# Performance work log

Measured on AMD Instinct MI355X. Metric: run time of the kernel, lower is better.

Reference implementation:

```python
import jax, jax.numpy as jnp
import numpy as np
import math

NUM_BANDS = 16
BINS = 1024
CROPSIZE = 1024
BATCH = 4


def setup_inputs() -> dict:
    key = jax.random.key(0)
    ks = jax.random.split(key, 10)
    s = 1.0 / math.sqrt(BINS)
    return {
        "x": jax.random.normal(ks[0], (BATCH, CROPSIZE, BINS), jnp.float32),
        "Wq": jax.random.normal(ks[1], (BINS, BINS), jnp.float32) * s,
        "bq": jax.random.normal(ks[2], (BINS,), jnp.float32) * 0.02,
        "Wk": jax.random.normal(ks[3], (BINS, BINS), jnp.float32) * s,
        "bk": jax.random.normal(ks[4], (BINS,), jnp.float32) * 0.02,
        "Wv": jax.random.normal(ks[5], (BINS, BINS), jnp.float32) * s,
        "bv": jax.random.normal(ks[6], (BINS,), jnp.float32) * 0.02,
        "Wo": jax.random.normal(ks[7], (BINS, BINS), jnp.float32) * s,
        "bo": jax.random.normal(ks[8], (BINS,), jnp.float32) * 0.02,
        "er": jax.random.normal(ks[9], (BINS // NUM_BANDS, CROPSIZE), jnp.float32),
    }


def reference(x, Wq, bq, Wk, bk, Wv, bv, Wo, bo, er):
    b, w, c = x.shape
    h = NUM_BANDS
    d = c // h
    # Linear projections (torch Linear: x @ W.T + b)
    q = (jnp.einsum("bwc,oc->bwo", x, Wq) + bq).reshape(b, w, h, d).transpose(0, 2, 1, 3)  # [b,h,w,d]
    k = (jnp.einsum("bwc,oc->bwo", x, Wk) + bk).reshape(b, w, h, d).transpose(0, 2, 1, 3)  # [b,h,w,d]
    v = (jnp.einsum("bwc,oc->bwo", x, Wv) + bv).reshape(b, w, h, d).transpose(0, 2, 1, 3)  # [b,h,w,d]
    # relative-position bias via skew trick
    qe = jnp.einsum("bhwd,dc->bhwc", q, er)  # [b,h,w,cropsize]
    qe = jnp.pad(qe, ((0, 0), (0, 0), (0, 0), (1, 0)))  # pad last dim on left -> [b,h,w,crop+1]
    p = jnp.swapaxes(qe, 2, 3)[:, :, 1:, :]  # [b,h,crop,w] == [b,h,w,w] since crop==w
    qk = (jnp.einsum("bhwd,bhud->bhwu", q, k) + p) / math.sqrt(c)
    a = jax.nn.softmax(qk, axis=-1)
    av = jnp.einsum("bhwu,bhud->bhwd", a, v).transpose(0, 2, 1, 3).reshape(b, w, c)
    return jnp.einsum("bwc,oc->bwo", av, Wo) + bo
```

## Files before the change

### kernel.cpp

```cpp
#include <hip/hip_runtime.h>
#include <stdint.h>

typedef __attribute__((ext_vector_type(8))) short   short8;
typedef __attribute__((ext_vector_type(8))) __bf16  bf16x8;
typedef __attribute__((ext_vector_type(4))) float   floatx4;

__device__ __forceinline__ float bf2f(uint16_t h) {
    union { uint32_t u; float f; } v; v.u = ((uint32_t)h) << 16; return v.f;
}
__device__ __forceinline__ uint16_t f2bf(float f) {
    union { float f; uint32_t u; } v; v.f = f;
    uint32_t u = v.u;
    u += 0x7FFFu + ((u >> 16) & 1u);
    return (uint16_t)(u >> 16);
}
__device__ __forceinline__ floatx4 mfma16(short8 a, short8 b, floatx4 c) {
    return __builtin_amdgcn_mfma_f32_16x16x32_bf16(
        __builtin_bit_cast(bf16x8, a), __builtin_bit_cast(bf16x8, b), c, 0, 0, 0);
}
__device__ __forceinline__ void gll16(const short* g, short* l) {
    __builtin_amdgcn_global_load_lds(
        (const __attribute__((address_space(1))) uint32_t*)g,
        (__attribute__((address_space(3))) uint32_t*)l, 16, 0, 0);
}

__global__ void conv_all(
    const float* __restrict__ x,
    const float* __restrict__ Wq, const float* __restrict__ Wk,
    const float* __restrict__ Wv, const float* __restrict__ Wo,
    const float* __restrict__ bq, const float* __restrict__ bk,
    const float* __restrict__ bv, const float* __restrict__ bo,
    const float* __restrict__ er,
    short* __restrict__ xb, short* __restrict__ Wb,
    short* __restrict__ ball, short* __restrict__ ErT)
{
    int blk = blockIdx.x, tid = threadIdx.x;
    if (blk < 4096) {
        int i = blk * 256 + tid;
        float4 v = ((const float4*)x)[i];
        ((short4*)xb)[i] = make_short4((short)f2bf(v.x), (short)f2bf(v.y),
                                       (short)f2bf(v.z), (short)f2bf(v.w));
    } else if (blk < 8192) {
        int rel = blk - 4096;
        int wsel = rel >> 10;
        int i = (rel & 1023) * 256 + tid;
        const float* W = (wsel == 0) ? Wq : (wsel == 1) ? Wk : (wsel == 2) ? Wv : Wo;
        float4 v = ((const float4*)W)[i];
        ((short4*)(Wb + ((size_t)wsel << 20)))[i] =
            make_short4((short)f2bf(v.x), (short)f2bf(v.y),
                        (short)f2bf(v.z), (short)f2bf(v.w));
    } else if (blk < 8448) {
        int idx = (blk - 8192) * 256 + tid;
        int w = idx >> 6, d = idx & 63;
        ErT[idx] = (short)f2bf(er[d * 1024 + w]);
    } else {
        int idx = (blk - 8448) * 256 + tid;
        int sel = idx >> 10, j = idx & 1023;
        const float* s = (sel == 0) ? bq : (sel == 1) ? bk : (sel == 2) ? bv : bo;
        ball[idx] = (short)f2bf(s[j]);
    }
}

__device__ __forceinline__ void gemm_body(
    const short* __restrict__ A, const short* __restrict__ Wt,
    const short* __restrict__ bias, short* __restrict__ dst,
    float* __restrict__ dstf, int variant)
{
    __shared__ short As[128 * 64];
    __shared__ short Bs[128 * 64];
    const int tid  = threadIdx.x;
    const int wid  = tid >> 6;
    const int lane = tid & 63;
    const int m0 = blockIdx.x * 128;
    const int n0 = blockIdx.y * 128;
    const int wm = (wid >> 1) * 64;
    const int wn = (wid & 1) * 64;
    const int lrow = lane & 15;
    const int quad = lane >> 4;
    const int srow = lane >> 3;
    const int sscol = (((lane & 7) ^ (srow & 7)) << 3);
    const int rx = lrow & 7;

    floatx4 acc[4][4];
#pragma unroll
    for (int r = 0; r < 4; ++r)
#pragma unroll
        for (int c = 0; c < 4; ++c) acc[r][c] = (floatx4){0.f, 0.f, 0.f, 0.f};

    for (int k0 = 0; k0 < 1024; k0 += 64) {
#pragma unroll
        for (int i = 0; i < 4; ++i) {
            int q = wid * 4 + i;
            gll16(A + (size_t)(m0 + q * 8 + srow) * 1024 + k0 + sscol,
                  &As[q * 512 + lane * 8]);
        }
#pragma unroll
        for (int i = 0; i < 4; ++i) {
            int q = wid * 4 + i;
            gll16(Wt + (size_t)(n0 + q * 8 + srow) * 1024 + k0 + sscol,
                  &Bs[q * 512 + lane * 8]);
        }
        __syncthreads();
#pragma unroll
        for (int ks = 0; ks < 2; ++ks) {
            short8 af[4], bfr[4];
#pragma unroll
            for (int r = 0; r < 4; ++r)
                af[r] = *(const short8*)&As[(wm + r * 16 + lrow) * 64 +
                                            (((ks * 4 + quad) ^ rx) << 3)];
#pragma unroll
            for (int c = 0; c < 4; ++c)
                bfr[c] = *(const short8*)&Bs[(wn + c * 16 + lrow) * 64 +
                                             (((ks * 4 + quad) ^ rx) << 3)];
#pragma unroll
            for (int r = 0; r < 4; ++r)
#pragma unroll
                for (int c = 0; c < 4; ++c)
                    acc[r][c] = mfma16(af[r], bfr[c], acc[r][c]);
        }
        __syncthreads();
    }

#pragma unroll
    for (int c = 0; c < 4; ++c) {
        int col = n0 + wn + c * 16 + lrow;
        float bv = bf2f((uint16_t)bias[col]);
#pragma unroll
        for (int r = 0; r < 4; ++r) {
#pragma unroll
            for (int g = 0; g < 4; ++g) {
                int m = m0 + wm + r * 16 + quad * 4 + g;
                float fv = acc[r][c][g] + bv;
                if (variant == 3) {
                    dstf[(size_t)m * 1024 + col] = fv;
                } else if (variant == 2) {
                    int bh = (m >> 10) * 16 + (col >> 6);
                    dst[(size_t)bh * 65536 + (size_t)(col & 63) * 1024 + (m & 1023)] =
                        (short)f2bf(fv);
                } else {
                    int bh = (m >> 10) * 16 + (col >> 6);
                    dst[(size_t)bh * 65536 + (size_t)(m & 1023) * 64 + (col & 63)] =
                        (short)f2bf(fv);
                }
            }
        }
    }
}

__global__ __launch_bounds__(256) void qkv_gemm(
    const short* __restrict__ x,
    const short* __restrict__ Wb, const short* __restrict__ bqkv,
    short* __restrict__ Qb, short* __restrict__ Kb, short* __restrict__ Vb)
{
    int z = blockIdx.z;
    const short* Wt = Wb + ((size_t)z << 20);
    short* dst      = (z == 0) ? Qb : (z == 1) ? Kb : Vb;
    gemm_body(x, Wt, bqkv + z * 1024, dst, nullptr, z);
}

__global__ __launch_bounds__(256) void out_gemm(
    const short* __restrict__ AV, const short* __restrict__ Wo,
    const short* __restrict__ bo, float* __restrict__ out)
{
    gemm_body(AV, Wo, bo, nullptr, out, 3);
}

#define PSTR 72
__global__ __launch_bounds__(512) void attn_kernel(
    const short* __restrict__ Q, const short* __restrict__ K,
    const short* __restrict__ Vt, const short* __restrict__ ErT,
    short* __restrict__ AV)
{
    __shared__ short Ks [2][64 * 64];
    __shared__ short Qks[2][64 * 64];
    __shared__ short Vs [2][64 * 64];
    __shared__ short Ps [128 * PSTR];
    const int tid  = threadIdx.x;
    const int wid  = tid >> 6;
    const int lane = tid & 63;
    const int lrow = lane & 15;
    const int quad = lane >> 4;
    const int lk   = quad * 8;
    const int srow = lane >> 3;
    const int sscol = (((lane & 7) ^ (srow & 7)) << 3);
    const int rx = lrow & 7;
    const int h = blockIdx.x, b = blockIdx.y;
    const int bh = b * 16 + h;
    const int i0 = blockIdx.z * 128;
    const int wrow = wid * 16;
    const short* Qbh = Q  + (size_t)bh * 65536;
    const short* Kbh = K  + (size_t)bh * 65536;
    const short* Vbh = Vt + (size_t)bh * 65536;

    short8 qa[4];
    {
        int row = i0 + wrow + lrow;
#pragma unroll
        for (int kk = 0; kk < 2; ++kk) {
            qa[kk]     = *(const short8*)&Qbh[(size_t)row * 64 + kk * 32 + lk];
            qa[kk + 2] = *(const short8*)&ErT[(size_t)row * 64 + kk * 32 + lk];
        }
    }

    float lrun[4];
    floatx4 oacc[4];
#pragma unroll
    for (int g = 0; g < 4; ++g) lrun[g] = 0.f;
#pragma unroll
    for (int c = 0; c < 4; ++c) oacc[c] = (floatx4){0.f, 0.f, 0.f, 0.f};

    {
        gll16(Kbh + (size_t)(wid * 8 + srow) * 64 + sscol,    &Ks [0][wid * 512 + lane * 8]);
        gll16(Qbh + (size_t)(wid * 8 + srow) * 64 + sscol,    &Qks[0][wid * 512 + lane * 8]);
        gll16(Vbh + (size_t)(wid * 8 + srow) * 1024 + sscol,  &Vs [0][wid * 512 + lane * 8]);
    }

    const float sc2 = 1.44269504088896f / 32.0f;

    for (int jt = 0; jt < 16; ++jt) {
        const int cur = jt & 1;
        __syncthreads();

        if (jt < 15) {
            int j1 = (jt + 1) * 64;
            gll16(Kbh + (size_t)(j1 + wid * 8 + srow) * 64 + sscol,    &Ks [cur ^ 1][wid * 512 + lane * 8]);
            gll16(Qbh + (size_t)(j1 + wid * 8 + srow) * 64 + sscol,    &Qks[cur ^ 1][wid * 512 + lane * 8]);
            gll16(Vbh + (size_t)(wid * 8 + srow) * 1024 + j1 + sscol,  &Vs [cur ^ 1][wid * 512 + lane * 8]);
        }

        floatx4 s[4];
#pragma unroll
        for (int c = 0; c < 4; ++c) s[c] = (floatx4){0.f, 0.f, 0.f, 0.f};
#pragma unroll
        for (int kk = 0; kk < 4; ++kk) {
            short8 kb[4];
#pragma unroll
            for (int c = 0; c < 4; ++c) {
                int kl = (kk < 2) ? kk : kk - 2;
                const short* src = (kk < 2) ? Ks[cur] : Qks[cur];
                kb[c] = *(const short8*)&src[(c * 16 + lrow) * 64 +
                                             (((kl * 4 + quad) ^ rx) << 3)];
            }
#pragma unroll
            for (int c = 0; c < 4; ++c)
                s[c] = mfma16(qa[kk], kb[c], s[c]);
        }

#pragma unroll
        for (int c = 0; c < 4; ++c)
#pragma unroll
            for (int g = 0; g < 4; ++g)
                s[c][g] = exp2f(s[c][g] * sc2);
#pragma unroll
        for (int g = 0; g < 4; ++g) {
            float rs = (s[0][g] + s[1][g]) + (s[2][g] + s[3][g]);
#pragma unroll
            for (int d = 1; d < 16; d <<= 1) rs += __shfl_xor(rs, d, 64);
            lrun[g] += rs;
        }

#pragma unroll
        for (int c = 0; c < 4; ++c)
#pragma unroll
            for (int g = 0; g < 4; ++g)
                Ps[(wrow + quad * 4 + g) * PSTR + c * 16 + lrow] = (short)f2bf(s[c][g]);
        __asm__ __volatile__("" ::: "memory");

#pragma unroll
        for (int kk = 0; kk < 2; ++kk) {
            short8 pa, vb[4];
            pa = *(const short8*)&Ps[(wrow + lrow) * PSTR + kk * 32 + lk];
#pragma unroll
            for (int c = 0; c < 4; ++c)
                vb[c] = *(const short8*)&Vs[cur][(c * 16 + lrow) * 64 +
                                                 (((kk * 4 + quad) ^ rx) << 3)];
#pragma unroll
            for (int c = 0; c < 4; ++c)
                oacc[c] = mfma16(pa, vb[c], oacc[c]);
        }
    }

#pragma unroll
    for (int c = 0; c < 4; ++c)
#pragma unroll
        for (int g = 0; g < 4; ++g) {
            int row = i0 + wrow + quad * 4 + g;
            int colc = h * 64 + c * 16 + lrow;
            AV[((size_t)b * 1024 + row) * 1024 + colc] = (short)f2bf(oacc[c][g] / lrun[g]);
        }
}

extern "C" void kernel_launch(void* const* d_in, const int* in_sizes, int n_in,
                              void* d_out, int out_size, void* d_ws, size_t ws_size,
                              hipStream_t stream) {
    const float* x  = (const float*)d_in[0];
    const float* Wq = (const float*)d_in[1];
    const float* bq = (const float*)d_in[2];
    const float* Wk = (const float*)d_in[3];
    const float* bk = (const float*)d_in[4];
    const float* Wv = (const float*)d_in[5];
    const float* bv = (const float*)d_in[6];
    const float* Wo = (const float*)d_in[7];
    const float* bo = (const float*)d_in[8];
    const float* er = (const float*)d_in[9];
    float* out = (float*)d_out;

    const size_t M1 = 1u << 20;
    short* ws   = (short*)d_ws;
    short* xb   = (short*)d_out;
    short* Qb   = ws;
    short* Kb   = ws + 4 * M1;
    short* Vb   = ws + 8 * M1;
    short* AVb  = ws + 12 * M1;
    short* Wb   = ws + 16 * M1;
    short* ball = ws + 20 * M1;
    short* ErT  = ws + 20 * M1 + 4096;

    hipLaunchKernelGGL(conv_all, dim3(8464), dim3(256), 0, stream,
                       x, Wq, Wk, Wv, Wo, bq, bk, bv, bo, er, xb, Wb, ball, ErT);
    hipLaunchKernelGGL(qkv_gemm, dim3(32, 8, 3), dim3(256), 0, stream,
                       xb, Wb, ball, Qb, Kb, Vb);
    hipLaunchKernelGGL(attn_kernel, dim3(16, 4, 8), dim3(512), 0, stream,
                       Qb, Kb, Vb, ErT, AVb);
    hipLaunchKernelGGL(out_gemm, dim3(32, 8), dim3(256), 0, stream,
                       AVb, Wb + 3 * M1, ball + 3072, out);
}
```

Measured before the change: 213.9 us.

## Replace QKV GEMM with 256x256-tile 8-wave pipelined kernel

Replaces the QKV projection GEMM with a new kernel that uses 256x256 output tiles, 512 threads, and 128KB dynamic LDS. Global-to-LDS loads are double-buffered and interleaved with MFMA quadrants, with explicit barriers, vmcnt waits, and setprio. The aim is more operand reuse per tile and hidden load latency. The cost is 192 blocks on 256 CUs, which leaves some CUs idle, plus heavy register pressure and many barriers.

```diff
diff --git a/kernel.cpp b/kernel.cpp
--- a/kernel.cpp
+++ b/kernel.cpp
@@ -147,22 +147,160 @@
     }
 }
 
-__global__ __launch_bounds__(256) void qkv_gemm(
-    const short* __restrict__ x,
-    const short* __restrict__ Wb, const short* __restrict__ bqkv,
-    short* __restrict__ Qb, short* __restrict__ Kb, short* __restrict__ Vb)
-{
-    int z = blockIdx.z;
-    const short* Wt = Wb + ((size_t)z << 20);
-    short* dst      = (z == 0) ? Qb : (z == 1) ? Kb : Vb;
-    gemm_body(x, Wt, bqkv + z * 1024, dst, nullptr, z);
-}
-
 __global__ __launch_bounds__(256) void out_gemm(
     const short* __restrict__ AV, const short* __restrict__ Wo,
     const short* __restrict__ bo, float* __restrict__ out)
 {
     gemm_body(AV, Wo, bo, nullptr, out, 3);
+}
+
+#define Q8_BAR   asm volatile("s_barrier" ::: "memory")
+#define Q8_VM4   asm volatile("s_waitcnt vmcnt(4)" ::: "memory")
+#define Q8_VM0   asm volatile("s_waitcnt vmcnt(0)" ::: "memory")
+
+__device__ __forceinline__ void stage_half(const short* src, short* region, int tid)
+{
+    const int lane = tid & 63;
+    const int wid  = tid >> 6;
+    const int srow = lane >> 3;
+    const int scol = (((lane & 7) ^ srow) << 3);
+#pragma unroll
+    for (int round = 0; round < 2; ++round) {
+        int r = round * 64 + wid * 8 + srow;
+        gll16(src + (size_t)r * 1024 + scol,
+              region + round * 4096 + wid * 512 + lane * 8);
+    }
+}
+
+#define SA(buf, h) (As + ((buf) * 2 + (h)) * 8192)
+#define SB(buf, h) (Bs + ((buf) * 2 + (h)) * 8192)
+#define STAGE_A(buf, h, kt) stage_half(Asrc + (size_t)(h) * 131072 + (size_t)(kt) * 64, SA(buf, h), tid)
+#define STAGE_B(buf, h, kt) stage_half(Bsrc + (size_t)(h) * 131072 + (size_t)(kt) * 64, SB(buf, h), tid)
+
+#define READ_A(buf, MQ) do { const short* Rp_ = SA(buf, wm); \
+    _Pragma("unroll") for (int r_ = 0; r_ < 4; ++r_) { \
+        int row_ = (MQ) * 64 + r_ * 16 + lrow; \
+        _Pragma("unroll") for (int ks_ = 0; ks_ < 2; ++ks_) \
+            a[r_][ks_] = *(const short8*)&Rp_[row_ * 64 + (((ks_ * 4 + quad) ^ rx) << 3)]; \
+    } } while (0)
+
+#define READ_B(buf, NQ, BB) do { const short* Rp_ = SB(buf, wn >> 1); \
+    _Pragma("unroll") for (int c_ = 0; c_ < 2; ++c_) { \
+        int row_ = (wn & 1) * 64 + (NQ) * 32 + c_ * 16 + lrow; \
+        _Pragma("unroll") for (int ks_ = 0; ks_ < 2; ++ks_) \
+            BB[c_][ks_] = *(const short8*)&Rp_[row_ * 64 + (((ks_ * 4 + quad) ^ rx) << 3)]; \
+    } } while (0)
+
+#define MFMA_QUAD(MQ, NQ, BB) do { \
+    __builtin_amdgcn_s_setprio(1); \
+    _Pragma("unroll") for (int ks_ = 0; ks_ < 2; ++ks_) \
+        _Pragma("unroll") for (int r_ = 0; r_ < 4; ++r_) \
+            _Pragma("unroll") for (int c_ = 0; c_ < 2; ++c_) \
+                acc[(MQ) * 4 + r_][(NQ) * 2 + c_] = \
+                    mfma16(a[r_][ks_], BB[c_][ks_], acc[(MQ) * 4 + r_][(NQ) * 2 + c_]); \
+    __builtin_amdgcn_s_setprio(0); \
+    } while (0)
+
+__global__ __launch_bounds__(512, 2) void qkv_gemm256(
+    const short* __restrict__ x, const short* __restrict__ Wb,
+    const short* __restrict__ ball,
+    short* __restrict__ Qb, short* __restrict__ Kb, short* __restrict__ Vb)
+{
+    extern __shared__ short lds[];
+    short* As = lds;
+    short* Bs = lds + 32768;
+    const int tid  = threadIdx.x;
+    const int wid  = tid >> 6;
+    const int lane = tid & 63;
+    const int wm   = wid >> 2;
+    const int wn   = wid & 3;
+    const int lrow = lane & 15;
+    const int quad = lane >> 4;
+    const int rx   = lrow & 7;
+    const int m0 = blockIdx.x * 256;
+    const int n0 = blockIdx.y * 256;
+    const short* Asrc = x  + (size_t)m0 * 1024;
+    const short* Bsrc = Wb + (size_t)n0 * 1024;
+
+    floatx4 acc[8][4];
+#pragma unroll
+    for (int r = 0; r < 8; ++r)
+#pragma unroll
+        for (int c = 0; c < 4; ++c) acc[r][c] = (floatx4){0.f, 0.f, 0.f, 0.f};
+
+    short8 a[4][2], b0[2][2], b1[2][2];
+
+    STAGE_A(0, 0, 0); STAGE_A(0, 1, 0); STAGE_B(0, 0, 0); STAGE_B(0, 1, 0);
+    STAGE_B(1, 0, 1); STAGE_B(1, 1, 1);
+    Q8_VM4;
+    Q8_BAR;
+
+#pragma unroll 1
+    for (int i = 0; i < 7; ++i) {
+        const int t1 = 2 * i + 1, s0 = 2 * i + 2, s1 = 2 * i + 3;
+        READ_A(0, 0); READ_B(0, 0, b0);
+        STAGE_A(1, 0, t1);
+        Q8_BAR; MFMA_QUAD(0, 0, b0); Q8_BAR;
+        READ_B(0, 1, b1);
+        STAGE_A(1, 1, t1);
+        Q8_BAR; MFMA_QUAD(0, 1, b1); Q8_BAR;
+        READ_A(0, 1);
+        STAGE_B(0, 0, s0);
+        Q8_BAR; MFMA_QUAD(1, 1, b1); Q8_BAR;
+        STAGE_B(0, 1, s0);
+        Q8_VM4;
+        Q8_BAR; MFMA_QUAD(1, 0, b0); Q8_BAR;
+        READ_A(1, 0); READ_B(1, 0, b0);
+        STAGE_A(0, 0, s0);
+        Q8_BAR; MFMA_QUAD(0, 0, b0); Q8_BAR;
+        READ_B(1, 1, b1);
+        STAGE_A(0, 1, s0);
+        Q8_BAR; MFMA_QUAD(0, 1, b1); Q8_BAR;
+        READ_A(1, 1);
+        STAGE_B(1, 0, s1);
+        Q8_BAR; MFMA_QUAD(1, 1, b1); Q8_BAR;
+        STAGE_B(1, 1, s1);
+        Q8_VM4;
+        Q8_BAR; MFMA_QUAD(1, 0, b0); Q8_BAR;
+    }
+
+    STAGE_A(1, 0, 15); STAGE_A(1, 1, 15);
+    Q8_VM4;
+    Q8_BAR;
+    READ_A(0, 0); READ_B(0, 0, b0); READ_B(0, 1, b1);
+    MFMA_QUAD(0, 0, b0); MFMA_QUAD(0, 1, b1);
+    READ_A(0, 1);
+    MFMA_QUAD(1, 0, b0); MFMA_QUAD(1, 1, b1);
+    Q8_VM0;
+    Q8_BAR;
+    READ_A(1, 0); READ_B(1, 0, b0); READ_B(1, 1, b1);
+    MFMA_QUAD(0, 0, b0); MFMA_QUAD(0, 1, b1);
+    READ_A(1, 1);
+    MFMA_QUAD(1, 0, b0); MFMA_QUAD(1, 1, b1);
+
+    const int z = n0 >> 10;
+    short* dst = (z == 0) ? Qb : (z == 1) ? Kb : Vb;
+#pragma unroll
+    for (int fc = 0; fc < 4; ++fc) {
+        int col = n0 + wn * 64 + fc * 16 + lrow;
+        int c1  = col & 1023;
+        float bv = bf2f((uint16_t)ball[col]);
+#pragma unroll
+        for (int fr = 0; fr < 8; ++fr) {
+#pragma unroll
+            for (int g = 0; g < 4; ++g) {
+                int m = m0 + wm * 128 + fr * 16 + quad * 4 + g;
+                float fv = acc[fr][fc][g] + bv;
+                int bh = (m >> 10) * 16 + (c1 >> 6);
+                if (z == 2)
+                    dst[(size_t)bh * 65536 + (size_t)(c1 & 63) * 1024 + (m & 1023)] =
+                        (short)f2bf(fv);
+                else
+                    dst[(size_t)bh * 65536 + (size_t)(m & 1023) * 64 + (c1 & 63)] =
+                        (short)f2bf(fv);
+            }
+        }
+    }
 }
 
 #define PSTR 72
@@ -316,9 +454,16 @@
     short* ball = ws + 20 * M1;
     short* ErT  = ws + 20 * M1 + 4096;
 
+    static bool attr_done = false;
+    if (!attr_done) {
+        hipFuncSetAttribute((const void*)qkv_gemm256,
+                            hipFuncAttributeMaxDynamicSharedMemorySize, 131072);
+        attr_done = true;
+    }
+
     hipLaunchKernelGGL(conv_all, dim3(8464), dim3(256), 0, stream,
                        x, Wq, Wk, Wv, Wo, bq, bk, bv, bo, er, xb, Wb, ball, ErT);
-    hipLaunchKernelGGL(qkv_gemm, dim3(32, 8, 3), dim3(256), 0, stream,
+    hipLaunchKernelGGL(qkv_gemm256, dim3(16, 12), dim3(512), 131072, stream,
                        xb, Wb, ball, Qb, Kb, Vb);
     hipLaunchKernelGGL(attn_kernel, dim3(16, 4, 8), dim3(512), 0, stream,
                        Qb, Kb, Vb, ErT, AVb);
```

Result: no change. 217.6 us (+1.7%).

## Replace QKV GEMM with 256x192-tile pipelined kernel using direct-to-LDS loads

Applied to the files above, without the earlier changes.

Replaces the per-projection QKV GEMM (grid 32x8x3, 256 threads) with one fused 256x192-tile kernel of 512 threads. It treats the three weight matrices as a single N=3072 problem and launches 256 blocks with a swizzled block order. K-slices are double-buffered in LDS through global_load_lds with XOR swizzling. Manual vmcnt waits and barriers overlap staging of the next slice with MFMA phases, and setprio raises priority during math. The aim is more data reuse per tile, fewer blocks, and better load/compute overlap; the costs are 112KB of dynamic LDS, high register pressure and hand-tuned wait counts.

```diff
diff --git a/kernel.cpp b/kernel.cpp
--- a/kernel.cpp
+++ b/kernel.cpp
@@ -147,22 +147,142 @@
     }
 }
 
-__global__ __launch_bounds__(256) void qkv_gemm(
-    const short* __restrict__ x,
-    const short* __restrict__ Wb, const short* __restrict__ bqkv,
-    short* __restrict__ Qb, short* __restrict__ Kb, short* __restrict__ Vb)
-{
-    int z = blockIdx.z;
-    const short* Wt = Wb + ((size_t)z << 20);
-    short* dst      = (z == 0) ? Qb : (z == 1) ? Kb : Vb;
-    gemm_body(x, Wt, bqkv + z * 1024, dst, nullptr, z);
-}
-
 __global__ __launch_bounds__(256) void out_gemm(
     const short* __restrict__ AV, const short* __restrict__ Wo,
     const short* __restrict__ bo, float* __restrict__ out)
 {
     gemm_body(AV, Wo, bo, nullptr, out, 3);
+}
+
+#define VM7  asm volatile("s_waitcnt vmcnt(7)" ::: "memory")
+#define VM6  asm volatile("s_waitcnt vmcnt(6)" ::: "memory")
+#define VM0  asm volatile("s_waitcnt vmcnt(0)" ::: "memory")
+#define BARR asm volatile("s_barrier" ::: "memory")
+
+__device__ __forceinline__ void stage_unit(const short* src, short* region, int tid)
+{
+    const int row  = tid >> 3;
+    const int scol = (((tid & 7) ^ (row & 7)) << 3);
+    gll16(src + (size_t)row * 1024 + scol, region + tid * 8);
+}
+
+#define SAU(buf, u) (As + (buf) * 16384 + (u) * 4096)
+#define SBU(buf, u) (Bs + (buf) * 12288 + (u) * 4096)
+#define STG_A(buf, u, kt) stage_unit(Asrc + (size_t)(u) * 65536 + (size_t)(kt) * 64, SAU(buf, u), tid)
+#define STG_B(buf, u, kt) stage_unit(Bsrc + (size_t)(u) * 65536 + (size_t)(kt) * 64, SBU(buf, u), tid)
+
+#define RD_A(buf) do { \
+    _Pragma("unroll") for (int fr_ = 0; fr_ < 8; ++fr_) { \
+        const short* p_ = SAU(buf, wm * 2 + (fr_ >> 2)) + ((fr_ & 3) * 16 + lrow) * 64; \
+        _Pragma("unroll") for (int ks_ = 0; ks_ < 2; ++ks_) \
+            a[fr_][ks_] = *(const short8*)&p_[((ks_ * 4 + quad) ^ rx) << 3]; \
+    } } while (0)
+
+#define RD_B(buf, c) do { \
+    const short* p_ = SBU(buf, c) + (wn * 16 + lrow) * 64; \
+    _Pragma("unroll") for (int ks_ = 0; ks_ < 2; ++ks_) \
+        bb[ks_] = *(const short8*)&p_[((ks_ * 4 + quad) ^ rx) << 3]; \
+    } while (0)
+
+#define MFMA_PH(c) do { \
+    __builtin_amdgcn_s_setprio(1); \
+    _Pragma("unroll") for (int ks_ = 0; ks_ < 2; ++ks_) \
+        _Pragma("unroll") for (int fr_ = 0; fr_ < 8; ++fr_) \
+            acc[fr_][c] = mfma16(a[fr_][ks_], bb[ks_], acc[fr_][c]); \
+    __builtin_amdgcn_s_setprio(0); \
+    } while (0)
+
+__global__ __launch_bounds__(512, 2) void qkv_gemm192(
+    const short* __restrict__ x, const short* __restrict__ Wb,
+    const short* __restrict__ ball,
+    short* __restrict__ Qb, short* __restrict__ Kb, short* __restrict__ Vb)
+{
+    extern __shared__ short lds[];
+    short* As = lds;
+    short* Bs = lds + 32768;
+    const int tid  = threadIdx.x;
+    const int wid  = tid >> 6;
+    const int lane = tid & 63;
+    const int wm   = wid >> 2;
+    const int wn   = wid & 3;
+    const int lrow = lane & 15;
+    const int quad = lane >> 4;
+    const int rx   = lrow & 7;
+    const int bid  = blockIdx.x;
+    const int swz  = (bid & 7) * 32 + (bid >> 3);
+    const int mi   = swz & 15, ni = swz >> 4;
+    const int m0   = mi * 256, n0 = ni * 192;
+    const short* Asrc = x  + (size_t)m0 * 1024;
+    const short* Bsrc = Wb + (size_t)n0 * 1024;
+
+    floatx4 acc[8][3];
+#pragma unroll
+    for (int r = 0; r < 8; ++r)
+#pragma unroll
+        for (int c = 0; c < 3; ++c) acc[r][c] = (floatx4){0.f, 0.f, 0.f, 0.f};
+
+    short8 a[8][2], bb[2];
+
+    STG_A(0, 0, 0); STG_A(0, 1, 0); STG_A(0, 2, 0); STG_A(0, 3, 0);
+    STG_B(0, 0, 0); STG_B(0, 1, 0); STG_B(0, 2, 0);
+    STG_A(1, 0, 1); STG_A(1, 1, 1); STG_A(1, 2, 1); STG_A(1, 3, 1);
+    STG_B(1, 0, 1); STG_B(1, 1, 1);
+    VM6; BARR;
+
+#pragma unroll 1
+    for (int i = 0; i < 7; ++i) {
+        const int t1 = 2 * i + 1, s0 = 2 * i + 2, s1 = 2 * i + 3;
+        STG_B(1, 2, t1);
+        VM7; BARR;
+        RD_A(0); RD_B(0, 0); MFMA_PH(0);
+        BARR;
+        STG_A(0, 0, s0); STG_A(0, 1, s0); STG_B(0, 0, s0);
+        BARR; RD_B(0, 1); MFMA_PH(1); BARR;
+        STG_A(0, 2, s0); STG_A(0, 3, s0); STG_B(0, 1, s0);
+        BARR; RD_B(0, 2); MFMA_PH(2); BARR;
+        STG_B(0, 2, s0);
+        VM7; BARR;
+        RD_A(1); RD_B(1, 0); MFMA_PH(0);
+        BARR;
+        STG_A(1, 0, s1); STG_A(1, 1, s1); STG_B(1, 0, s1);
+        BARR; RD_B(1, 1); MFMA_PH(1); BARR;
+        STG_A(1, 2, s1); STG_A(1, 3, s1); STG_B(1, 1, s1);
+        BARR; RD_B(1, 2); MFMA_PH(2); BARR;
+    }
+
+    STG_B(1, 2, 15);
+    VM7; BARR;
+    RD_A(0); RD_B(0, 0); MFMA_PH(0);
+    RD_B(0, 1); MFMA_PH(1);
+    RD_B(0, 2); MFMA_PH(2);
+    VM0; BARR;
+    RD_A(1); RD_B(1, 0); MFMA_PH(0);
+    RD_B(1, 1); MFMA_PH(1);
+    RD_B(1, 2); MFMA_PH(2);
+
+#pragma unroll
+    for (int fc = 0; fc < 3; ++fc) {
+        int col = n0 + fc * 64 + wn * 16 + lrow;
+        int z   = col >> 10;
+        int c1  = col & 1023;
+        short* dst = (z == 0) ? Qb : (z == 1) ? Kb : Vb;
+        float bv = bf2f((uint16_t)ball[col]);
+#pragma unroll
+        for (int fr = 0; fr < 8; ++fr) {
+#pragma unroll
+            for (int g = 0; g < 4; ++g) {
+                int m = m0 + wm * 128 + fr * 16 + quad * 4 + g;
+                float fv = acc[fr][fc][g] + bv;
+                int bh = (m >> 10) * 16 + (c1 >> 6);
+                if (z == 2)
+                    dst[(size_t)bh * 65536 + (size_t)(c1 & 63) * 1024 + (m & 1023)] =
+                        (short)f2bf(fv);
+                else
+                    dst[(size_t)bh * 65536 + (size_t)(m & 1023) * 64 + (c1 & 63)] =
+                        (short)f2bf(fv);
+            }
+        }
+    }
 }
 
 #define PSTR 72
@@ -316,9 +436,16 @@
     short* ball = ws + 20 * M1;
     short* ErT  = ws + 20 * M1 + 4096;
 
+    static bool attr_done = false;
+    if (!attr_done) {
+        hipFuncSetAttribute((const void*)qkv_gemm192,
+                            hipFuncAttributeMaxDynamicSharedMemorySize, 114688);
+        attr_done = true;
+    }
+
     hipLaunchKernelGGL(conv_all, dim3(8464), dim3(256), 0, stream,
                        x, Wq, Wk, Wv, Wo, bq, bk, bv, bo, er, xb, Wb, ball, ErT);
-    hipLaunchKernelGGL(qkv_gemm, dim3(32, 8, 3), dim3(256), 0, stream,
+    hipLaunchKernelGGL(qkv_gemm192, dim3(256), dim3(512), 114688, stream,
                        xb, Wb, ball, Qb, Kb, Vb);
     hipLaunchKernelGGL(attn_kernel, dim3(16, 4, 8), dim3(512), 0, stream,
                        Qb, Kb, Vb, ErT, AVb);
```

After: 209.4 us. -2.1%, faster.
